# Optimization experiments

Measured on AMD Instinct MI355X. Metric: run time of the kernel, lower is better.

Reference implementation:

```python
import jax, jax.numpy as jnp
import numpy as np

B, L, D_MODEL, H = 4, 2048, 1024, 16
HD = D_MODEL // H
EPS = 1e-6


def setup_inputs() -> dict:
    key = jax.random.key(0)
    ks = jax.random.split(key, 9)
    s = 1.0 / np.sqrt(D_MODEL)
    return {
        "x": jax.random.normal(ks[0], (B, L, D_MODEL), dtype=jnp.float32),
        "Wq": jax.random.normal(ks[1], (D_MODEL, D_MODEL), dtype=jnp.float32) * s,
        "bq": jax.random.normal(ks[2], (D_MODEL,), dtype=jnp.float32) * 0.01,
        "Wk": jax.random.normal(ks[3], (D_MODEL, D_MODEL), dtype=jnp.float32) * s,
        "bk": jax.random.normal(ks[4], (D_MODEL,), dtype=jnp.float32) * 0.01,
        "Wv": jax.random.normal(ks[5], (D_MODEL, D_MODEL), dtype=jnp.float32) * s,
        "bv": jax.random.normal(ks[6], (D_MODEL,), dtype=jnp.float32) * 0.01,
        "Wo": jax.random.normal(ks[7], (D_MODEL, D_MODEL), dtype=jnp.float32) * s,
        "bo": jax.random.normal(ks[8], (D_MODEL,), dtype=jnp.float32) * 0.01,
    }


def reference(x, Wq, bq, Wk, bk, Wv, bv, Wo, bo):
    b, l, _ = x.shape
    s = l  # self-attention: keys length == queries length

    def proj(W, bias):
        # [B, L, d_model] -> [B, H, L, head_dim]
        return (x @ W.T + bias).reshape(b, l, H, HD).transpose(0, 2, 1, 3)

    q = jax.nn.sigmoid(proj(Wq, bq))  # kernel feature map
    k = jax.nn.sigmoid(proj(Wk, bk))
    v = proj(Wv, bv)

    # flow conservation normalizations (per head, per position)
    sink_incoming = 1.0 / jnp.einsum('nhld,nhd->nhl', q + EPS, k.sum(axis=2) + EPS)
    source_outgoing = 1.0 / jnp.einsum('nhld,nhd->nhl', k + EPS, q.sum(axis=2) + EPS)
    conserved_sink = jnp.einsum(
        'nhld,nhd->nhl', q + EPS, (k * source_outgoing[..., None]).sum(axis=2) + EPS)
    conserved_source = jnp.einsum(
        'nhld,nhd->nhl', k + EPS, (q * sink_incoming[..., None]).sum(axis=2) + EPS)
    conserved_source = jnp.clip(conserved_source, -1.0, 1.0)

    sink_allocation = jax.nn.sigmoid(conserved_sink * (float(l) / float(s)))
    source_competition = jax.nn.softmax(conserved_source, axis=-1) * float(s)

    # linear-attention kv trick: (q') @ (k^T v')
    kv = jnp.einsum('nhld,nhlm->nhdm', k, v * source_competition[..., None])
    out = jnp.einsum('nhld,nhdm->nhlm', q * sink_incoming[..., None], kv)
    out = out * sink_allocation[..., None]

    out = out.transpose(0, 2, 1, 3).reshape(b, l, D_MODEL)
    return out @ Wo.T + bo  # dropout is identity in eval
```

## Files before the change

### kernel.cpp

```cpp
#include <hip/hip_runtime.h>
#include <math.h>

#define B_ 4
#define L_ 2048
#define DM 1024
#define H_ 16
#define HD_ 64
#define NH_ 64
#define EPS_ 1e-6f

typedef float f32x4 __attribute__((ext_vector_type(4)));
typedef _Float16 half8 __attribute__((ext_vector_type(8)));
typedef _Float16 half4 __attribute__((ext_vector_type(4)));

typedef __attribute__((address_space(3))) void lds_v;
typedef const __attribute__((address_space(1))) void glb_v;
#define GLOAD16(g, l) __builtin_amdgcn_global_load_lds((glb_v*)(g), (lds_v*)(l), 16, 0, 0)

__device__ __forceinline__ float sigmoidf_(float x) { return 1.0f / (1.0f + expf(-x)); }

__global__ __launch_bounds__(256) void splitx_kernel(
    const float* __restrict__ in, _Float16* __restrict__ outp, int n4)
{
    const int i = blockIdx.x * 256 + threadIdx.x;
    if (i >= n4) return;
    f32x4 v = *(const f32x4*)(in + (size_t)i * 4);
    half4 h = { (_Float16)v[0], (_Float16)v[1], (_Float16)v[2], (_Float16)v[3] };
    *(half4*)(outp + (size_t)i * 4) = h;
}

__global__ __launch_bounds__(256) void split_w4_kernel(
    const float* __restrict__ Wq, const float* __restrict__ Wk,
    const float* __restrict__ Wv, const float* __restrict__ Wo,
    _Float16* __restrict__ wh3, _Float16* __restrict__ woh,
    float* __restrict__ sums)
{
    const int y = blockIdx.y;
    if (y == 0 && blockIdx.x < 64)
        sums[blockIdx.x * 256 + threadIdx.x] = 0.f;
    const float* src = (y == 0) ? Wq : (y == 1) ? Wk : (y == 2) ? Wv : Wo;
    _Float16* hh = (y < 3) ? (wh3 + (size_t)y * DM * DM) : woh;
    const int i = blockIdx.x * 256 + threadIdx.x;
    f32x4 v = *(const f32x4*)(src + (size_t)i * 4);
    half4 h = { (_Float16)v[0], (_Float16)v[1], (_Float16)v[2], (_Float16)v[3] };
    *(half4*)(hh + (size_t)i * 4) = h;
}

__global__ __launch_bounds__(256) void gemm_qkv_kernel(
    const _Float16* __restrict__ xf,
    const _Float16* __restrict__ wh,
    const float* __restrict__ bq, const float* __restrict__ bk, const float* __restrict__ bv,
    _Float16* __restrict__ qb, _Float16* __restrict__ kb, _Float16* __restrict__ vb,
    float* __restrict__ qsum, float* __restrict__ ksum)
{
    const int bid = (int)blockIdx.x;
    const int wg = (bid & 7) * 192 + (bid >> 3);
    const int z = wg / 512;
    const int rem = wg & 511;
    const int row0 = (rem >> 3) * 128;
    const int col0 = (rem & 7) * 128;
    const float* __restrict__ bias  = (z == 0) ? bq : (z == 1) ? bk : bv;
    _Float16* __restrict__ outp     = (z == 0) ? qb : (z == 1) ? kb : vb;
    const _Float16* Wh = wh + (size_t)z * DM * DM;

    __shared__ _Float16 lds[2 * 8192];
    const int t = threadIdx.x;
    const int lane = t & 63;
    const int w = t >> 6;
    const int wr = w >> 1, wc = w & 1;
    const int fr = lane & 15, kc = lane >> 4;

    f32x4 acc[4][4];
    #pragma unroll
    for (int m = 0; m < 4; ++m)
        #pragma unroll
        for (int n = 0; n < 4; ++n) acc[m][n] = f32x4{0.f, 0.f, 0.f, 0.f};

    for (int k0 = 0; k0 < DM; k0 += 64) {
        const _Float16* a_g = xf + (size_t)row0 * DM + k0;
        const _Float16* b_g = Wh + (size_t)col0 * DM + k0;
        #pragma unroll
        for (int p = 0; p < 4; ++p) {
            const int b = p * 4096 + t * 16;
            const int r = b >> 7;
            const int s = (b >> 4) & 7;
            const int c = ((s ^ (r & 7)) << 3);
            const size_t go = (size_t)r * DM + c;
            GLOAD16(a_g + go, lds + (b >> 1));
            GLOAD16(b_g + go, lds + 8192 + (b >> 1));
        }
        __syncthreads();

        #pragma unroll
        for (int ks = 0; ks < 2; ++ks) {
            const int sl = (ks << 2) | kc;
            half8 bf[4];
            #pragma unroll
            for (int n = 0; n < 4; ++n) {
                const int row = wc * 64 + n * 16 + fr;
                bf[n] = *(const half8*)(lds + 8192 + row * 64 + ((sl ^ (row & 7)) << 3));
            }
            #pragma unroll
            for (int m = 0; m < 4; ++m) {
                const int row = wr * 64 + m * 16 + fr;
                half8 af = *(const half8*)(lds + row * 64 + ((sl ^ (row & 7)) << 3));
                #pragma unroll
                for (int n = 0; n < 4; ++n)
                    acc[m][n] = __builtin_amdgcn_mfma_f32_16x16x32_f16(af, bf[n], acc[m][n], 0, 0, 0);
            }
        }
        __syncthreads();
    }

    float csum[4] = {0.f, 0.f, 0.f, 0.f};
    #pragma unroll
    for (int m = 0; m < 4; ++m) {
        const int gr0 = row0 + wr * 64 + m * 16 + kc * 4;
        #pragma unroll
        for (int n = 0; n < 4; ++n) {
            const int j = col0 + wc * 64 + n * 16 + fr;
            const float bj = bias[j];
            const int h = j >> 6, dd = j & 63;
            #pragma unroll
            for (int r2 = 0; r2 < 4; ++r2) {
                const int i = gr0 + r2;
                const int nn = i >> 11, l = i & (L_ - 1);
                float v = acc[m][n][r2] + bj;
                if (z < 2) { v = sigmoidf_(v); csum[n] += v; }
                outp[(((size_t)(nn * H_ + h)) * L_ + l) * HD_ + dd] = (_Float16)v;
            }
        }
    }

    if (z < 2) {
        float* scol = (float*)lds;
        if (t < 128) scol[t] = 0.f;
        __syncthreads();
        #pragma unroll
        for (int n = 0; n < 4; ++n)
            atomicAdd(&scol[wc * 64 + n * 16 + fr], csum[n]);
        __syncthreads();
        if (t < 128) {
            const int j = col0 + t;
            const int nn = row0 >> 11;
            float* dst = (z == 0) ? qsum : ksum;
            atomicAdd(&dst[(nn * H_ + (j >> 6)) * 64 + (j & 63)], scol[t]);
        }
    }
}

__global__ __launch_bounds__(256) void gemm_out_kernel(
    const _Float16* __restrict__ af, const _Float16* __restrict__ wo,
    const float* __restrict__ bias, float* __restrict__ outp)
{
    const int bid = (int)blockIdx.x;
    const int wg = (bid & 7) * 64 + (bid >> 3);
    const int row0 = (wg >> 3) * 128;
    const int col0 = (wg & 7) * 128;

    __shared__ _Float16 lds[2 * 8192];
    const int t = threadIdx.x;
    const int lane = t & 63;
    const int w = t >> 6;
    const int wr = w >> 1, wc = w & 1;
    const int fr = lane & 15, kc = lane >> 4;

    f32x4 acc[4][4];
    #pragma unroll
    for (int m = 0; m < 4; ++m)
        #pragma unroll
        for (int n = 0; n < 4; ++n) acc[m][n] = f32x4{0.f, 0.f, 0.f, 0.f};

    for (int k0 = 0; k0 < DM; k0 += 64) {
        const _Float16* a_g = af + (size_t)row0 * DM + k0;
        const _Float16* b_g = wo + (size_t)col0 * DM + k0;
        #pragma unroll
        for (int p = 0; p < 4; ++p) {
            const int b = p * 4096 + t * 16;
            const int r = b >> 7;
            const int s = (b >> 4) & 7;
            const int c = ((s ^ (r & 7)) << 3);
            const size_t go = (size_t)r * DM + c;
            GLOAD16(a_g + go, lds + (b >> 1));
            GLOAD16(b_g + go, lds + 8192 + (b >> 1));
        }
        __syncthreads();

        #pragma unroll
        for (int ks = 0; ks < 2; ++ks) {
            const int sl = (ks << 2) | kc;
            half8 bf[4];
            #pragma unroll
            for (int n = 0; n < 4; ++n) {
                const int row = wc * 64 + n * 16 + fr;
                bf[n] = *(const half8*)(lds + 8192 + row * 64 + ((sl ^ (row & 7)) << 3));
            }
            #pragma unroll
            for (int m = 0; m < 4; ++m) {
                const int row = wr * 64 + m * 16 + fr;
                half8 af8 = *(const half8*)(lds + row * 64 + ((sl ^ (row & 7)) << 3));
                #pragma unroll
                for (int n = 0; n < 4; ++n)
                    acc[m][n] = __builtin_amdgcn_mfma_f32_16x16x32_f16(af8, bf[n], acc[m][n], 0, 0, 0);
            }
        }
        __syncthreads();
    }

    #pragma unroll
    for (int m = 0; m < 4; ++m) {
        const int gr0 = row0 + wr * 64 + m * 16 + kc * 4;
        #pragma unroll
        for (int n = 0; n < 4; ++n) {
            const int j = col0 + wc * 64 + n * 16 + fr;
            const float bj = bias[j];
            #pragma unroll
            for (int r2 = 0; r2 < 4; ++r2)
                outp[(size_t)(gr0 + r2) * DM + j] = acc[m][n][r2] + bj;
        }
    }
}

__global__ __launch_bounds__(256) void stage1_kernel(
    const _Float16* __restrict__ q, const _Float16* __restrict__ k,
    const float* __restrict__ qsum, const float* __restrict__ ksum,
    float* __restrict__ si, float* __restrict__ qsi, float* __restrict__ kso)
{
    const int nh = blockIdx.x, ch = blockIdx.y;
    const _Float16* qp = q + (size_t)nh * L_ * HD_;
    const _Float16* kp = k + (size_t)nh * L_ * HD_;
    const int tid = threadIdx.x;
    const int lane = tid & 63;
    const int w = tid >> 6;
    const int r8 = lane >> 3;
    const int oct = lane & 7;

    __shared__ float ksum_s[64], qsum_s[64];
    __shared__ float s1[4][64], s2[4][64];
    if (tid < 64) {
        ksum_s[tid] = ksum[nh * 64 + tid] + EPS_;
        qsum_s[tid] = qsum[nh * 64 + tid] + EPS_;
    }
    __syncthreads();

    float qacc[8] = {0.f}, kacc[8] = {0.f};
    #pragma unroll
    for (int it = 0; it < 8; ++it) {
        const int l = ch * 256 + it * 32 + w * 8 + r8;
        half8 q8 = *(const half8*)(qp + (size_t)l * HD_ + oct * 8);
        half8 k8 = *(const half8*)(kp + (size_t)l * HD_ + oct * 8);
        float a = 0.f, b = 0.f;
        #pragma unroll
        for (int j = 0; j < 8; ++j) {
            a += ((float)q8[j] + EPS_) * ksum_s[oct * 8 + j];
            b += ((float)k8[j] + EPS_) * qsum_s[oct * 8 + j];
        }
        a += __shfl_xor(a, 1); a += __shfl_xor(a, 2); a += __shfl_xor(a, 4);
        b += __shfl_xor(b, 1); b += __shfl_xor(b, 2); b += __shfl_xor(b, 4);
        const float siv = 1.f / a;
        const float sov = 1.f / b;
        if (oct == 0) si[nh * L_ + l] = siv;
        #pragma unroll
        for (int j = 0; j < 8; ++j) {
            qacc[j] += (float)q8[j] * siv;
            kacc[j] += (float)k8[j] * sov;
        }
    }
    #pragma unroll
    for (int j = 0; j < 8; ++j) {
        qacc[j] += __shfl_xor(qacc[j], 8);  qacc[j] += __shfl_xor(qacc[j], 16); qacc[j] += __shfl_xor(qacc[j], 32);
        kacc[j] += __shfl_xor(kacc[j], 8);  kacc[j] += __shfl_xor(kacc[j], 16); kacc[j] += __shfl_xor(kacc[j], 32);
    }
    if (r8 == 0) {
        #pragma unroll
        for (int j = 0; j < 8; ++j) { s1[w][oct * 8 + j] = qacc[j]; s2[w][oct * 8 + j] = kacc[j]; }
    }
    __syncthreads();
    if (tid < 64) {
        atomicAdd(&qsi[nh * 64 + tid], s1[0][tid] + s1[1][tid] + s1[2][tid] + s1[3][tid]);
        atomicAdd(&kso[nh * 64 + tid], s2[0][tid] + s2[1][tid] + s2[2][tid] + s2[3][tid]);
    }
}

__global__ __launch_bounds__(256) void kv_part_kernel(
    const _Float16* __restrict__ k, const _Float16* __restrict__ v,
    const float* __restrict__ qsi, float* __restrict__ kvp, float* __restrict__ psum_p)
{
    const int nh = blockIdx.x, ch = blockIdx.y;
    const _Float16* kp = k + (size_t)nh * L_ * HD_;
    const _Float16* vp = v + (size_t)nh * L_ * HD_;
    const int tid = threadIdx.x;
    const int lane = tid & 63;
    const int w = tid >> 6;
    const int row8 = tid >> 3;
    const int oct = tid & 7;

    __shared__ float qsi_s[64];
    __shared__ float ks[32][65], vs[32][65];
    __shared__ float pl[32];
    if (tid < 64) qsi_s[tid] = qsi[nh * 64 + tid] + EPS_;
    __syncthreads();

    float acc[16] = {0.f};
    float psum_acc = 0.f;
    for (int l0 = ch * 256; l0 < (ch + 1) * 256; l0 += 32) {
        {
            const half8* kp8 = (const half8*)(kp + (size_t)l0 * HD_);
            const half8* vp8 = (const half8*)(vp + (size_t)l0 * HD_);
            half8 k8 = kp8[tid];
            half8 v8 = vp8[tid];
            const int r = tid >> 3, c = (tid & 7) * 8;
            #pragma unroll
            for (int j = 0; j < 8; ++j) {
                ks[r][c + j] = (float)k8[j];
                vs[r][c + j] = (float)v8[j];
            }
        }
        __syncthreads();
        {
            float b = 0.f;
            #pragma unroll
            for (int j = 0; j < 8; ++j)
                b += (ks[row8][oct * 8 + j] + EPS_) * qsi_s[oct * 8 + j];
            b += __shfl_xor(b, 1); b += __shfl_xor(b, 2); b += __shfl_xor(b, 4);
            b = fminf(1.f, fmaxf(-1.f, b));
            const float p = expf(b);
            if (oct == 0) { pl[row8] = p; psum_acc += p; }
        }
        __syncthreads();
        #pragma unroll 4
        for (int ll = 0; ll < 32; ++ll) {
            const float vv = vs[ll][lane] * pl[ll];
            #pragma unroll
            for (int dd = 0; dd < 16; ++dd) acc[dd] += ks[ll][w * 16 + dd] * vv;
        }
        __syncthreads();
    }
    #pragma unroll
    for (int dd = 0; dd < 16; ++dd)
        kvp[((size_t)(nh * 8 + ch) * 64 + (w * 16 + dd)) * 64 + lane] = acc[dd];

    psum_acc += __shfl_xor(psum_acc, 8);
    psum_acc += __shfl_xor(psum_acc, 16);
    psum_acc += __shfl_xor(psum_acc, 32);
    psum_acc += __shfl_xor(psum_acc, 1);
    psum_acc += __shfl_xor(psum_acc, 2);
    psum_acc += __shfl_xor(psum_acc, 4);
    __shared__ float sp[4];
    if (lane == 0) sp[w] = psum_acc;
    __syncthreads();
    if (tid == 0) psum_p[nh * 8 + ch] = sp[0] + sp[1] + sp[2] + sp[3];
}

__global__ __launch_bounds__(256) void kv_reduce_kernel(
    const float* __restrict__ kvp, const float* __restrict__ psum_p,
    float* __restrict__ kvb)
{
    const int nh = blockIdx.x;
    float tot = 0.f;
    #pragma unroll
    for (int c = 0; c < 8; ++c) tot += psum_p[nh * 8 + c];
    const float scale = (float)L_ / tot;
    for (int e = threadIdx.x; e < 4096; e += 256) {
        float s = 0.f;
        #pragma unroll
        for (int c = 0; c < 8; ++c) s += kvp[(size_t)(nh * 8 + c) * 4096 + e];
        kvb[(size_t)nh * 4096 + e] = s * scale;
    }
}

__global__ __launch_bounds__(256) void out_kernel(
    const _Float16* __restrict__ q, const float* __restrict__ kvb,
    const float* __restrict__ si, const float* __restrict__ kso,
    _Float16* __restrict__ attn_f)
{
    const int nh = blockIdx.x;
    const int n = nh >> 4;
    const int h = nh & 15;
    const int l0 = blockIdx.y * 64;
    __shared__ float kvs[64][64];
    __shared__ float qs[64][65];
    __shared__ float sal[64];
    __shared__ float kso_s[64];
    const int tid = threadIdx.x;
    for (int i = tid; i < 4096; i += 256)
        kvs[i >> 6][i & 63] = kvb[(size_t)nh * 4096 + i];
    {
        const half8* src8 = (const half8*)(q + ((size_t)nh * L_ + l0) * HD_);
        for (int i = tid; i < 512; i += 256) {
            half8 v8 = src8[i];
            const int r = i >> 3, c = (i & 7) * 8;
            #pragma unroll
            for (int j = 0; j < 8; ++j) qs[r][c + j] = (float)v8[j];
        }
    }
    if (tid < 64) kso_s[tid] = kso[nh * 64 + tid] + EPS_;
    __syncthreads();
    {
        const int row = tid >> 3;
        const int oct = tid & 7;
        #pragma unroll
        for (int rr = 0; rr < 2; ++rr) {
            const int r = rr * 32 + row;
            float a = 0.f;
            #pragma unroll
            for (int j = 0; j < 8; ++j)
                a += (qs[r][oct * 8 + j] + EPS_) * kso_s[oct * 8 + j];
            a += __shfl_xor(a, 1); a += __shfl_xor(a, 2); a += __shfl_xor(a, 4);
            if (oct == 0) sal[r] = sigmoidf_(a);
        }
    }
    __syncthreads();
    const int lane = tid & 63;
    const int w = tid >> 6;
    for (int ll = w; ll < 64; ll += 4) {
        const int l = l0 + ll;
        float acc = 0.f;
        #pragma unroll
        for (int d = 0; d < 64; ++d) acc += qs[ll][d] * kvs[d][lane];
        const float val = acc * si[nh * L_ + l] * sal[ll];
        attn_f[((size_t)n * L_ + l) * DM + h * 64 + lane] = (_Float16)val;
    }
}

extern "C" void kernel_launch(void* const* d_in, const int* in_sizes, int n_in,
                              void* d_out, int out_size, void* d_ws, size_t ws_size,
                              hipStream_t stream)
{
    const float* x  = (const float*)d_in[0];
    const float* Wq = (const float*)d_in[1];
    const float* bq = (const float*)d_in[2];
    const float* Wk = (const float*)d_in[3];
    const float* bk = (const float*)d_in[4];
    const float* Wv = (const float*)d_in[5];
    const float* bv = (const float*)d_in[6];
    const float* Wo = (const float*)d_in[7];
    const float* bo = (const float*)d_in[8];
    float* out = (float*)d_out;

    float* ws = (float*)d_ws;
    size_t off = 0;
    const size_t big = (size_t)B_ * L_ * DM;
    _Float16* qbuf = (_Float16*)(ws + off); off += big / 2;
    _Float16* kbuf = (_Float16*)(ws + off); off += big / 2;
    _Float16* vbuf = (_Float16*)(ws + off); off += big / 2;
    _Float16* xf = (_Float16*)(ws + off);
    _Float16* attn_f = xf;
    off += big / 2;
    _Float16* wh3 = (_Float16*)(ws + off); off += (size_t)3 * DM * DM / 2;
    _Float16* woh = (_Float16*)(ws + off); off += (size_t)DM * DM / 2;
    float* kvp    = ws + off; off += (size_t)NH_ * 8 * 64 * 64;
    float* kvb    = ws + off; off += (size_t)NH_ * 64 * 64;
    float* sums = ws + off;
    float* qsum = sums;
    float* ksum = sums + 1 * NH_ * 64;
    float* qsi  = sums + 2 * NH_ * 64;
    float* kso  = sums + 3 * NH_ * 64;
    off += 4 * NH_ * 64;
    float* psum_p = ws + off; off += NH_ * 8;
    float* si     = ws + off; off += NH_ * L_;

    splitx_kernel<<<big / 4 / 256, 256, 0, stream>>>(x, xf, (int)(big / 4));
    split_w4_kernel<<<dim3(DM * DM / 4 / 256, 4), 256, 0, stream>>>(
        Wq, Wk, Wv, Wo, wh3, woh, sums);

    gemm_qkv_kernel<<<1536, 256, 0, stream>>>(xf, wh3, bq, bk, bv,
                                              qbuf, kbuf, vbuf, qsum, ksum);

    stage1_kernel<<<dim3(NH_, 8), 256, 0, stream>>>(qbuf, kbuf, qsum, ksum, si, qsi, kso);

    kv_part_kernel<<<dim3(NH_, 8), 256, 0, stream>>>(kbuf, vbuf, qsi, kvp, psum_p);
    kv_reduce_kernel<<<NH_, 256, 0, stream>>>(kvp, psum_p, kvb);

    out_kernel<<<dim3(NH_, L_ / 64), 256, 0, stream>>>(qbuf, kvb, si, kso, attn_f);

    gemm_out_kernel<<<512, 256, 0, stream>>>(attn_f, woh, bo, out);
}
```

Measured before the change: 240.1 us.

## Double-buffer GEMM LDS tiles, merge prep kernels, atomically reduce KV partials

Both fp16 MFMA GEMMs now double-buffer their LDS tiles, issuing the global-to-LDS loads for the next K tile before computing the current one so load latency overlaps with MFMA work. The x and weight conversion kernels are merged into one prep kernel, which also zeroes the KV accumulator. The separate kv_reduce kernel is removed: kv_part atomically accumulates into the KV buffer, and out_kernel applies the L/sum scale itself. This saves two launches and the partial-buffer traffic, but doubles GEMM LDS use to 64KB per block, which may lower occupancy, and adds float atomic contention with non-deterministic summation order.

```diff
diff --git a/kernel.cpp b/kernel.cpp
--- a/kernel.cpp
+++ b/kernel.cpp
@@ -19,31 +19,32 @@
 
 __device__ __forceinline__ float sigmoidf_(float x) { return 1.0f / (1.0f + expf(-x)); }
 
-__global__ __launch_bounds__(256) void splitx_kernel(
-    const float* __restrict__ in, _Float16* __restrict__ outp, int n4)
-{
-    const int i = blockIdx.x * 256 + threadIdx.x;
-    if (i >= n4) return;
-    f32x4 v = *(const f32x4*)(in + (size_t)i * 4);
-    half4 h = { (_Float16)v[0], (_Float16)v[1], (_Float16)v[2], (_Float16)v[3] };
-    *(half4*)(outp + (size_t)i * 4) = h;
-}
-
-__global__ __launch_bounds__(256) void split_w4_kernel(
+__global__ __launch_bounds__(256) void prep_kernel(
+    const float* __restrict__ x,
     const float* __restrict__ Wq, const float* __restrict__ Wk,
     const float* __restrict__ Wv, const float* __restrict__ Wo,
-    _Float16* __restrict__ wh3, _Float16* __restrict__ woh,
-    float* __restrict__ sums)
-{
-    const int y = blockIdx.y;
-    if (y == 0 && blockIdx.x < 64)
-        sums[blockIdx.x * 256 + threadIdx.x] = 0.f;
-    const float* src = (y == 0) ? Wq : (y == 1) ? Wk : (y == 2) ? Wv : Wo;
-    _Float16* hh = (y < 3) ? (wh3 + (size_t)y * DM * DM) : woh;
-    const int i = blockIdx.x * 256 + threadIdx.x;
-    f32x4 v = *(const f32x4*)(src + (size_t)i * 4);
-    half4 h = { (_Float16)v[0], (_Float16)v[1], (_Float16)v[2], (_Float16)v[3] };
-    *(half4*)(hh + (size_t)i * 4) = h;
+    _Float16* __restrict__ xf, _Float16* __restrict__ wh3, _Float16* __restrict__ woh,
+    float* __restrict__ sums, float* __restrict__ kvb)
+{
+    const int bid = (int)blockIdx.x;
+    const int tid = threadIdx.x;
+    if (bid < 8192) {
+        const int i = bid * 256 + tid;
+        f32x4 v = *(const f32x4*)(x + (size_t)i * 4);
+        half4 h = { (_Float16)v[0], (_Float16)v[1], (_Float16)v[2], (_Float16)v[3] };
+        *(half4*)(xf + (size_t)i * 4) = h;
+        if (bid < 1024) kvb[bid * 256 + tid] = 0.f;
+        if (bid < 64)   sums[bid * 256 + tid] = 0.f;
+    } else {
+        const int r = bid - 8192;
+        const int y = r >> 10;
+        const int i = (r & 1023) * 256 + tid;
+        const float* src = (y == 0) ? Wq : (y == 1) ? Wk : (y == 2) ? Wv : Wo;
+        _Float16* hh = (y < 3) ? (wh3 + (size_t)y * DM * DM) : woh;
+        f32x4 v = *(const f32x4*)(src + (size_t)i * 4);
+        half4 h = { (_Float16)v[0], (_Float16)v[1], (_Float16)v[2], (_Float16)v[3] };
+        *(half4*)(hh + (size_t)i * 4) = h;
+    }
 }
 
 __global__ __launch_bounds__(256) void gemm_qkv_kernel(
@@ -63,22 +64,17 @@
     _Float16* __restrict__ outp     = (z == 0) ? qb : (z == 1) ? kb : vb;
     const _Float16* Wh = wh + (size_t)z * DM * DM;
 
-    __shared__ _Float16 lds[2 * 8192];
+    __shared__ _Float16 lds[2 * 16384];
     const int t = threadIdx.x;
     const int lane = t & 63;
     const int w = t >> 6;
     const int wr = w >> 1, wc = w & 1;
     const int fr = lane & 15, kc = lane >> 4;
 
-    f32x4 acc[4][4];
-    #pragma unroll
-    for (int m = 0; m < 4; ++m)
-        #pragma unroll
-        for (int n = 0; n < 4; ++n) acc[m][n] = f32x4{0.f, 0.f, 0.f, 0.f};
-
-    for (int k0 = 0; k0 < DM; k0 += 64) {
+    auto STAGE = [&](int k0, int buf) {
         const _Float16* a_g = xf + (size_t)row0 * DM + k0;
         const _Float16* b_g = Wh + (size_t)col0 * DM + k0;
+        _Float16* dst = lds + buf * 16384;
         #pragma unroll
         for (int p = 0; p < 4; ++p) {
             const int b = p * 4096 + t * 16;
@@ -86,11 +82,24 @@
             const int s = (b >> 4) & 7;
             const int c = ((s ^ (r & 7)) << 3);
             const size_t go = (size_t)r * DM + c;
-            GLOAD16(a_g + go, lds + (b >> 1));
-            GLOAD16(b_g + go, lds + 8192 + (b >> 1));
-        }
-        __syncthreads();
-
+            GLOAD16(a_g + go, dst + (b >> 1));
+            GLOAD16(b_g + go, dst + 8192 + (b >> 1));
+        }
+    };
+
+    f32x4 acc[4][4];
+    #pragma unroll
+    for (int m = 0; m < 4; ++m)
+        #pragma unroll
+        for (int n = 0; n < 4; ++n) acc[m][n] = f32x4{0.f, 0.f, 0.f, 0.f};
+
+    STAGE(0, 0);
+    __syncthreads();
+
+    for (int kt = 0; kt < 16; ++kt) {
+        if (kt + 1 < 16) STAGE((kt + 1) * 64, (kt + 1) & 1);
+        const _Float16* bufA = lds + (kt & 1) * 16384;
+        const _Float16* bufB = bufA + 8192;
         #pragma unroll
         for (int ks = 0; ks < 2; ++ks) {
             const int sl = (ks << 2) | kc;
@@ -98,12 +107,12 @@
             #pragma unroll
             for (int n = 0; n < 4; ++n) {
                 const int row = wc * 64 + n * 16 + fr;
-                bf[n] = *(const half8*)(lds + 8192 + row * 64 + ((sl ^ (row & 7)) << 3));
+                bf[n] = *(const half8*)(bufB + row * 64 + ((sl ^ (row & 7)) << 3));
             }
             #pragma unroll
             for (int m = 0; m < 4; ++m) {
                 const int row = wr * 64 + m * 16 + fr;
-                half8 af = *(const half8*)(lds + row * 64 + ((sl ^ (row & 7)) << 3));
+                half8 af = *(const half8*)(bufA + row * 64 + ((sl ^ (row & 7)) << 3));
                 #pragma unroll
                 for (int n = 0; n < 4; ++n)
                     acc[m][n] = __builtin_amdgcn_mfma_f32_16x16x32_f16(af, bf[n], acc[m][n], 0, 0, 0);
@@ -158,22 +167,17 @@
     const int row0 = (wg >> 3) * 128;
     const int col0 = (wg & 7) * 128;
 
-    __shared__ _Float16 lds[2 * 8192];
+    __shared__ _Float16 lds[2 * 16384];
     const int t = threadIdx.x;
     const int lane = t & 63;
     const int w = t >> 6;
     const int wr = w >> 1, wc = w & 1;
     const int fr = lane & 15, kc = lane >> 4;
 
-    f32x4 acc[4][4];
-    #pragma unroll
-    for (int m = 0; m < 4; ++m)
-        #pragma unroll
-        for (int n = 0; n < 4; ++n) acc[m][n] = f32x4{0.f, 0.f, 0.f, 0.f};
-
-    for (int k0 = 0; k0 < DM; k0 += 64) {
+    auto STAGE = [&](int k0, int buf) {
         const _Float16* a_g = af + (size_t)row0 * DM + k0;
         const _Float16* b_g = wo + (size_t)col0 * DM + k0;
+        _Float16* dst = lds + buf * 16384;
         #pragma unroll
         for (int p = 0; p < 4; ++p) {
             const int b = p * 4096 + t * 16;
@@ -181,11 +185,24 @@
             const int s = (b >> 4) & 7;
             const int c = ((s ^ (r & 7)) << 3);
             const size_t go = (size_t)r * DM + c;
-            GLOAD16(a_g + go, lds + (b >> 1));
-            GLOAD16(b_g + go, lds + 8192 + (b >> 1));
-        }
-        __syncthreads();
-
+            GLOAD16(a_g + go, dst + (b >> 1));
+            GLOAD16(b_g + go, dst + 8192 + (b >> 1));
+        }
+    };
+
+    f32x4 acc[4][4];
+    #pragma unroll
+    for (int m = 0; m < 4; ++m)
+        #pragma unroll
+        for (int n = 0; n < 4; ++n) acc[m][n] = f32x4{0.f, 0.f, 0.f, 0.f};
+
+    STAGE(0, 0);
+    __syncthreads();
+
+    for (int kt = 0; kt < 16; ++kt) {
+        if (kt + 1 < 16) STAGE((kt + 1) * 64, (kt + 1) & 1);
+        const _Float16* bufA = lds + (kt & 1) * 16384;
+        const _Float16* bufB = bufA + 8192;
         #pragma unroll
         for (int ks = 0; ks < 2; ++ks) {
             const int sl = (ks << 2) | kc;
@@ -193,12 +210,12 @@
             #pragma unroll
             for (int n = 0; n < 4; ++n) {
                 const int row = wc * 64 + n * 16 + fr;
-                bf[n] = *(const half8*)(lds + 8192 + row * 64 + ((sl ^ (row & 7)) << 3));
+                bf[n] = *(const half8*)(bufB + row * 64 + ((sl ^ (row & 7)) << 3));
             }
             #pragma unroll
             for (int m = 0; m < 4; ++m) {
                 const int row = wr * 64 + m * 16 + fr;
-                half8 af8 = *(const half8*)(lds + row * 64 + ((sl ^ (row & 7)) << 3));
+                half8 af8 = *(const half8*)(bufA + row * 64 + ((sl ^ (row & 7)) << 3));
                 #pragma unroll
                 for (int n = 0; n < 4; ++n)
                     acc[m][n] = __builtin_amdgcn_mfma_f32_16x16x32_f16(af8, bf[n], acc[m][n], 0, 0, 0);
@@ -284,7 +301,7 @@
 
 __global__ __launch_bounds__(256) void kv_part_kernel(
     const _Float16* __restrict__ k, const _Float16* __restrict__ v,
-    const float* __restrict__ qsi, float* __restrict__ kvp, float* __restrict__ psum_p)
+    const float* __restrict__ qsi, float* __restrict__ kvb, float* __restrict__ psum_p)
 {
     const int nh = blockIdx.x, ch = blockIdx.y;
     const _Float16* kp = k + (size_t)nh * L_ * HD_;
@@ -338,7 +355,7 @@
     }
     #pragma unroll
     for (int dd = 0; dd < 16; ++dd)
-        kvp[((size_t)(nh * 8 + ch) * 64 + (w * 16 + dd)) * 64 + lane] = acc[dd];
+        atomicAdd(&kvb[(size_t)nh * 4096 + (w * 16 + dd) * 64 + lane], acc[dd]);
 
     psum_acc += __shfl_xor(psum_acc, 8);
     psum_acc += __shfl_xor(psum_acc, 16);
@@ -352,26 +369,10 @@
     if (tid == 0) psum_p[nh * 8 + ch] = sp[0] + sp[1] + sp[2] + sp[3];
 }
 
-__global__ __launch_bounds__(256) void kv_reduce_kernel(
-    const float* __restrict__ kvp, const float* __restrict__ psum_p,
-    float* __restrict__ kvb)
-{
-    const int nh = blockIdx.x;
-    float tot = 0.f;
-    #pragma unroll
-    for (int c = 0; c < 8; ++c) tot += psum_p[nh * 8 + c];
-    const float scale = (float)L_ / tot;
-    for (int e = threadIdx.x; e < 4096; e += 256) {
-        float s = 0.f;
-        #pragma unroll
-        for (int c = 0; c < 8; ++c) s += kvp[(size_t)(nh * 8 + c) * 4096 + e];
-        kvb[(size_t)nh * 4096 + e] = s * scale;
-    }
-}
-
 __global__ __launch_bounds__(256) void out_kernel(
     const _Float16* __restrict__ q, const float* __restrict__ kvb,
     const float* __restrict__ si, const float* __restrict__ kso,
+    const float* __restrict__ psum_p,
     _Float16* __restrict__ attn_f)
 {
     const int nh = blockIdx.x;
@@ -383,6 +384,10 @@
     __shared__ float sal[64];
     __shared__ float kso_s[64];
     const int tid = threadIdx.x;
+    float tot = 0.f;
+    #pragma unroll
+    for (int c = 0; c < 8; ++c) tot += psum_p[nh * 8 + c];
+    const float scale = (float)L_ / tot;
     for (int i = tid; i < 4096; i += 256)
         kvs[i >> 6][i & 63] = kvb[(size_t)nh * 4096 + i];
     {
@@ -418,7 +423,7 @@
         float acc = 0.f;
         #pragma unroll
         for (int d = 0; d < 64; ++d) acc += qs[ll][d] * kvs[d][lane];
-        const float val = acc * si[nh * L_ + l] * sal[ll];
+        const float val = acc * si[nh * L_ + l] * sal[ll] * scale;
         attn_f[((size_t)n * L_ + l) * DM + h * 64 + lane] = (_Float16)val;
     }
 }
@@ -449,7 +454,6 @@
     off += big / 2;
     _Float16* wh3 = (_Float16*)(ws + off); off += (size_t)3 * DM * DM / 2;
     _Float16* woh = (_Float16*)(ws + off); off += (size_t)DM * DM / 2;
-    float* kvp    = ws + off; off += (size_t)NH_ * 8 * 64 * 64;
     float* kvb    = ws + off; off += (size_t)NH_ * 64 * 64;
     float* sums = ws + off;
     float* qsum = sums;
@@ -460,19 +464,16 @@
     float* psum_p = ws + off; off += NH_ * 8;
     float* si     = ws + off; off += NH_ * L_;
 
-    splitx_kernel<<<big / 4 / 256, 256, 0, stream>>>(x, xf, (int)(big / 4));
-    split_w4_kernel<<<dim3(DM * DM / 4 / 256, 4), 256, 0, stream>>>(
-        Wq, Wk, Wv, Wo, wh3, woh, sums);
+    prep_kernel<<<12288, 256, 0, stream>>>(x, Wq, Wk, Wv, Wo, xf, wh3, woh, sums, kvb);
 
     gemm_qkv_kernel<<<1536, 256, 0, stream>>>(xf, wh3, bq, bk, bv,
                                               qbuf, kbuf, vbuf, qsum, ksum);
 
     stage1_kernel<<<dim3(NH_, 8), 256, 0, stream>>>(qbuf, kbuf, qsum, ksum, si, qsi, kso);
 
-    kv_part_kernel<<<dim3(NH_, 8), 256, 0, stream>>>(kbuf, vbuf, qsi, kvp, psum_p);
-    kv_reduce_kernel<<<NH_, 256, 0, stream>>>(kvp, psum_p, kvb);
-
-    out_kernel<<<dim3(NH_, L_ / 64), 256, 0, stream>>>(qbuf, kvb, si, kso, attn_f);
+    kv_part_kernel<<<dim3(NH_, 8), 256, 0, stream>>>(kbuf, vbuf, qsi, kvb, psum_p);
+
+    out_kernel<<<dim3(NH_, L_ / 64), 256, 0, stream>>>(qbuf, kvb, si, kso, psum_p, attn_f);
 
     gemm_out_kernel<<<512, 256, 0, stream>>>(attn_f, woh, bo, out);
 }
```

After: 227.7 us. 1.05x faster.
